# Kernel tuning notes

Hardware: AMD Instinct MI355X
Metric: run time of the kernel (lower is better)

Reference implementation:

```python
import jax, jax.numpy as jnp
import numpy as np

N, TC, K, TK, D, V = 64, 256, 32, 64, 256, 32000


def setup_inputs() -> dict:
    key = jax.random.key(0)
    k1, k2, k3, k4 = jax.random.split(key, 4)
    src_tokens = jax.random.randint(k1, (N, TC), 0, V)
    know_tokens = jax.random.randint(k2, (N, K, TK), 0, V)
    ck_mask = jnp.ones((N, K), dtype=bool)
    cs_ids = jax.random.randint(k3, (N,), 0, K)
    embed = jax.random.normal(k4, (V, D), dtype=jnp.float32)
    return {
        "src_tokens": src_tokens,
        "know_tokens": know_tokens,
        "ck_mask": ck_mask,
        "cs_ids": cs_ids,
        "use_cs_ids": 0,
        "embed": embed,
    }


def reference(src_tokens, know_tokens, ck_mask, cs_ids, use_cs_ids, embed):
    d = embed.shape[1]
    # "transformer" stand-in: embedding lookup; pad token 0 defines ragged mask
    ctx_enc = embed[src_tokens]                         # [N,Tc,D]
    ctx_mask = src_tokens != 0                          # [N,Tc]
    know_enc = embed[know_tokens]                       # [N,K,Tk,D]
    know_mask = (know_tokens != 0) & ck_mask[:, :, None]  # [N,K,Tk]

    ctx_len = ctx_mask.sum(-1)                          # [N]
    know_len = know_mask.sum(-1)                        # [N,K]

    # ragged segment-sum pooling with sqrt(D * length) normalization
    ctx_use = (ctx_enc * ctx_mask[..., None]).sum(1)
    ctx_use = ctx_use / jnp.sqrt(d * jnp.maximum(ctx_len, 1).astype(ctx_use.dtype))[:, None]
    know_use = (know_enc * know_mask[..., None]).sum(2)
    know_use = know_use / jnp.sqrt(d * jnp.maximum(know_len, 1).astype(know_use.dtype))[..., None]

    # batched mv attention: score per knowledge sentence
    ck_attn = jnp.einsum('nkd,nd->nk', know_use, ctx_use)  # [N,K]

    if use_cs_ids:
        cs = cs_ids
    else:
        cs = jnp.argmax(jnp.where(ck_mask, ck_attn, -jnp.inf), axis=1)

    ck_attn = jnp.where(ck_mask, ck_attn, 0.0)          # padded like to_tensor_mask

    # gather selected knowledge span
    cs_enc = jnp.take_along_axis(know_enc, cs[:, None, None, None], axis=1)[:, 0]   # [N,Tk,D]
    cs_mask = jnp.take_along_axis(know_mask, cs[:, None, None], axis=1)[:, 0]       # [N,Tk]

    full_enc = jnp.concatenate([cs_enc, ctx_enc], axis=1)      # [N,Tk+Tc,D]
    full_mask = jnp.concatenate([cs_mask, ctx_mask], axis=1)   # [N,Tk+Tc]
    full_enc = full_enc * full_mask[..., None]                 # zero padding like to_tensor_mask
    return full_enc, full_mask, ck_attn
```

## Files before the change

### kernel.cpp

```cpp
#include <hip/hip_runtime.h>
#include <hip/hip_bf16.h>
#include <math.h>

#define N_  64
#define TC_ 256
#define K_  32
#define TK_ 64
#define D_  256
#define TF_ (TK_ + TC_)

__global__ void k0_zero(float* __restrict__ ctx_sum, int* __restrict__ ctx_len) {
    int idx = blockIdx.x * 256 + threadIdx.x;
    if (idx < N_ * D_) ctx_sum[idx] = 0.f;
    if (idx < N_)      ctx_len[idx] = 0;
}

__global__ __launch_bounds__(256) void k1_ctx(
        const int* __restrict__ src, const float* __restrict__ embed,
        float* __restrict__ out_enc, float* __restrict__ out_mask,
        float* __restrict__ ctx_sum, int* __restrict__ ctx_len) {
    const int n = blockIdx.x >> 3;
    const int c = blockIdx.x & 7;
    const int d = threadIdx.x;

    __shared__ int toks[32];
    if (d < 32) toks[d] = src[n * TC_ + c * 32 + d];
    __syncthreads();

    float acc = 0.f;
    #pragma unroll 4
    for (int tt = 0; tt < 32; ++tt) {
        const int tok = toks[tt];
        float v = 0.f;
        if (tok != 0) v = embed[(size_t)tok * D_ + d];
        out_enc[((size_t)n * TF_ + TK_ + c * 32 + tt) * D_ + d] = v;
        acc += v;
    }
    atomicAdd(&ctx_sum[n * D_ + d], acc);

    if (d < 32) {
        const int m = (toks[d] != 0);
        out_mask[n * TF_ + TK_ + c * 32 + d] = m ? 1.f : 0.f;
        if (m) atomicAdd(&ctx_len[n], 1);
    }
}

__global__ __launch_bounds__(256) void k2_know(
        const int* __restrict__ know, const int* __restrict__ ckm,
        const float* __restrict__ embed,
        const float* __restrict__ ctx_sum, const int* __restrict__ ctx_len,
        float* __restrict__ out_attn, float* __restrict__ ws_score) {
    const int n = blockIdx.x >> 5;
    const int k = blockIdx.x & (K_ - 1);
    const int d = threadIdx.x;

    __shared__ int   toks[TK_];
    __shared__ float red[4];

    const int ck = ckm[n * K_ + k];
    if (d < TK_) toks[d] = know[((size_t)n * K_ + k) * TK_ + d];
    __syncthreads();

    float acc = 0.f;
    if (ck) {
        #pragma unroll 8
        for (int t = 0; t < TK_; ++t) {
            const int tok = toks[t];
            if (tok != 0) acc += embed[(size_t)tok * D_ + d];
        }
    }

    int lk = 0;
    if (d < 64) {
        unsigned long long ball = __ballot(ck && (toks[d] != 0));
        lk = __popcll(ball);
    }

    float p = acc * ctx_sum[n * D_ + d];
    #pragma unroll
    for (int o = 32; o > 0; o >>= 1) p += __shfl_down(p, o, 64);
    if ((d & 63) == 0) red[d >> 6] = p;
    __syncthreads();

    if (d == 0) {
        const float dot = red[0] + red[1] + red[2] + red[3];
        int lc = ctx_len[n]; if (lc < 1) lc = 1;
        if (lk < 1) lk = 1;
        const float score =
            dot / (sqrtf((float)D_ * (float)lc) * sqrtf((float)D_ * (float)lk));
        out_attn[n * K_ + k] = ck ? score : 0.f;
        ws_score[n * K_ + k] = ck ? score : -INFINITY;
    }
}

__global__ __launch_bounds__(256) void k3_sel(
        const int* __restrict__ know, const int* __restrict__ ckm,
        const int* __restrict__ cs_ids, const int* __restrict__ use_flag,
        const float* __restrict__ embed, const float* __restrict__ ws_score,
        float* __restrict__ out_enc, float* __restrict__ out_mask) {
    const int n = blockIdx.x >> 2;
    const int c = blockIdx.x & 3;
    const int d = threadIdx.x;

    int cs = 0;
    if (use_flag[0]) {
        cs = cs_ids[n];
    } else {
        float best = -INFINITY;
        #pragma unroll
        for (int j = 0; j < K_; ++j) {
            const float s = ws_score[n * K_ + j];
            if (s > best) { best = s; cs = j; }
        }
    }
    const int ck = ckm[n * K_ + cs];

    __shared__ int toks[16];
    if (d < 16) toks[d] = know[((size_t)n * K_ + cs) * TK_ + c * 16 + d];
    __syncthreads();

    #pragma unroll
    for (int tt = 0; tt < 16; ++tt) {
        const int tok = toks[tt];
        const int m = ck && (tok != 0);
        float v = 0.f;
        if (m) v = embed[(size_t)tok * D_ + d];
        out_enc[((size_t)n * TF_ + c * 16 + tt) * D_ + d] = v;
    }
    if (d < 16) {
        const int m = ck && (toks[d] != 0);
        out_mask[n * TF_ + c * 16 + d] = m ? 1.f : 0.f;
    }
}

extern "C" void kernel_launch(void* const* d_in, const int* in_sizes, int n_in,
                              void* d_out, int out_size, void* d_ws, size_t ws_size,
                              hipStream_t stream) {
    const int*   src      = (const int*)d_in[0];
    const int*   know     = (const int*)d_in[1];
    const int*   ckm      = (const int*)d_in[2];
    const int*   cs_ids   = (const int*)d_in[3];
    const int*   use_flag = (const int*)d_in[4];
    const float* embed    = (const float*)d_in[5];

    float* out      = (float*)d_out;
    float* out_enc  = out;
    float* out_mask = out + (size_t)N_ * TF_ * D_;
    float* out_attn = out_mask + (size_t)N_ * TF_;

    float* ctx_sum  = (float*)d_ws;
    int*   ctx_len  = (int*)(ctx_sum + N_ * D_);
    float* ws_score = (float*)(ctx_len + N_);

    hipLaunchKernelGGL(k0_zero, dim3((N_ * D_ + 255) / 256), dim3(256), 0, stream,
                       ctx_sum, ctx_len);
    hipLaunchKernelGGL(k1_ctx, dim3(N_ * 8), dim3(256), 0, stream,
                       src, embed, out_enc, out_mask, ctx_sum, ctx_len);
    hipLaunchKernelGGL(k2_know, dim3(N_ * K_), dim3(256), 0, stream,
                       know, ckm, embed, ctx_sum, ctx_len, out_attn, ws_score);
    hipLaunchKernelGGL(k3_sel, dim3(N_ * 4), dim3(256), 0, stream,
                       know, ckm, cs_ids, use_flag, embed, ws_score,
                       out_enc, out_mask);
}
```

Before: 130.5 us.

## Vectorize embedding gathers with float4 and replace atomics with per-chunk partials

Embedding rows are now gathered and written as float4, with each wave handling a subset of tokens across all 64 float4 lanes of a row. The zeroing kernel and the atomicAdd accumulation of context sums and lengths are replaced by per-chunk partial sums in workspace, which the knowledge kernel reduces itself. This removes one launch and atomic contention, and cuts the number of memory instructions. The cost is that every knowledge block re-reads eight partial vectors, and there is an extra shared-memory reduction in the context kernel.

```diff
diff --git a/kernel.cpp b/kernel.cpp
--- a/kernel.cpp
+++ b/kernel.cpp
@@ -1,5 +1,4 @@
 #include <hip/hip_runtime.h>
-#include <hip/hip_bf16.h>
 #include <math.h>
 
 #define N_  64
@@ -7,100 +6,125 @@
 #define K_  32
 #define TK_ 64
 #define D_  256
+#define D4_ (D_ / 4)
 #define TF_ (TK_ + TC_)
 
-__global__ void k0_zero(float* __restrict__ ctx_sum, int* __restrict__ ctx_len) {
-    int idx = blockIdx.x * 256 + threadIdx.x;
-    if (idx < N_ * D_) ctx_sum[idx] = 0.f;
-    if (idx < N_)      ctx_len[idx] = 0;
-}
-
-__global__ __launch_bounds__(256) void k1_ctx(
-        const int* __restrict__ src, const float* __restrict__ embed,
-        float* __restrict__ out_enc, float* __restrict__ out_mask,
-        float* __restrict__ ctx_sum, int* __restrict__ ctx_len) {
+__global__ __launch_bounds__(256) void kA_ctx(
+        const int* __restrict__ src, const float4* __restrict__ embed4,
+        float4* __restrict__ out_enc4, float* __restrict__ out_mask,
+        float4* __restrict__ ws_part4, int* __restrict__ ws_clen) {
     const int n = blockIdx.x >> 3;
     const int c = blockIdx.x & 7;
-    const int d = threadIdx.x;
+    const int tid = threadIdx.x;
+    const int w = tid >> 6, l = tid & 63;
 
     __shared__ int toks[32];
-    if (d < 32) toks[d] = src[n * TC_ + c * 32 + d];
+    __shared__ float4 part[4][64];
+
+    if (tid < 32) {
+        const int tok = src[n * TC_ + c * 32 + tid];
+        toks[tid] = tok;
+        out_mask[n * TF_ + TK_ + c * 32 + tid] = tok ? 1.f : 0.f;
+    }
     __syncthreads();
 
-    float acc = 0.f;
-    #pragma unroll 4
-    for (int tt = 0; tt < 32; ++tt) {
-        const int tok = toks[tt];
-        float v = 0.f;
-        if (tok != 0) v = embed[(size_t)tok * D_ + d];
-        out_enc[((size_t)n * TF_ + TK_ + c * 32 + tt) * D_ + d] = v;
-        acc += v;
+    float4 acc = {0.f, 0.f, 0.f, 0.f};
+    #pragma unroll
+    for (int i = 0; i < 8; ++i) {
+        const int t = w * 8 + i;
+        const int tok = toks[t];
+        float4 v = {0.f, 0.f, 0.f, 0.f};
+        if (tok) v = embed4[(size_t)tok * D4_ + l];
+        out_enc4[((size_t)n * TF_ + TK_ + c * 32 + t) * D4_ + l] = v;
+        acc.x += v.x; acc.y += v.y; acc.z += v.z; acc.w += v.w;
     }
-    atomicAdd(&ctx_sum[n * D_ + d], acc);
+    part[w][l] = acc;
+    __syncthreads();
 
-    if (d < 32) {
-        const int m = (toks[d] != 0);
-        out_mask[n * TF_ + TK_ + c * 32 + d] = m ? 1.f : 0.f;
-        if (m) atomicAdd(&ctx_len[n], 1);
+    if (w == 0) {
+        float4 a = part[0][l], b = part[1][l], p2 = part[2][l], p3 = part[3][l];
+        a.x += b.x + p2.x + p3.x;
+        a.y += b.y + p2.y + p3.y;
+        a.z += b.z + p2.z + p3.z;
+        a.w += b.w + p2.w + p3.w;
+        ws_part4[(size_t)(n * 8 + c) * D4_ + l] = a;
+        const unsigned long long ball = __ballot(l < 32 && toks[l] != 0);
+        if (l == 0) ws_clen[n * 8 + c] = __popcll(ball);
     }
 }
 
-__global__ __launch_bounds__(256) void k2_know(
+__global__ __launch_bounds__(256) void kB_know(
         const int* __restrict__ know, const int* __restrict__ ckm,
-        const float* __restrict__ embed,
-        const float* __restrict__ ctx_sum, const int* __restrict__ ctx_len,
+        const float4* __restrict__ embed4,
+        const float4* __restrict__ ws_part4, const int* __restrict__ ws_clen,
         float* __restrict__ out_attn, float* __restrict__ ws_score) {
     const int n = blockIdx.x >> 5;
     const int k = blockIdx.x & (K_ - 1);
-    const int d = threadIdx.x;
+    const int tid = threadIdx.x;
+    const int w = tid >> 6, l = tid & 63;
 
-    __shared__ int   toks[TK_];
-    __shared__ float red[4];
+    __shared__ int toks[TK_];
+    __shared__ float redp[4];
+    __shared__ int lk_sh;
+
+    if (tid < TK_) toks[tid] = know[((size_t)n * K_ + k) * TK_ + tid];
+    __syncthreads();
 
     const int ck = ckm[n * K_ + k];
-    if (d < TK_) toks[d] = know[((size_t)n * K_ + k) * TK_ + d];
-    __syncthreads();
 
-    float acc = 0.f;
+    float4 ctx = {0.f, 0.f, 0.f, 0.f};
+    #pragma unroll
+    for (int c = 0; c < 8; ++c) {
+        const float4 v = ws_part4[(size_t)(n * 8 + c) * D4_ + l];
+        ctx.x += v.x; ctx.y += v.y; ctx.z += v.z; ctx.w += v.w;
+    }
+
+    float4 acc = {0.f, 0.f, 0.f, 0.f};
     if (ck) {
-        #pragma unroll 8
-        for (int t = 0; t < TK_; ++t) {
-            const int tok = toks[t];
-            if (tok != 0) acc += embed[(size_t)tok * D_ + d];
+        #pragma unroll
+        for (int i = 0; i < 16; ++i) {
+            const int tok = toks[w * 16 + i];
+            if (tok) {
+                const float4 v = embed4[(size_t)tok * D4_ + l];
+                acc.x += v.x; acc.y += v.y; acc.z += v.z; acc.w += v.w;
+            }
         }
     }
 
-    int lk = 0;
-    if (d < 64) {
-        unsigned long long ball = __ballot(ck && (toks[d] != 0));
-        lk = __popcll(ball);
-    }
-
-    float p = acc * ctx_sum[n * D_ + d];
+    float p = acc.x * ctx.x + acc.y * ctx.y + acc.z * ctx.z + acc.w * ctx.w;
     #pragma unroll
     for (int o = 32; o > 0; o >>= 1) p += __shfl_down(p, o, 64);
-    if ((d & 63) == 0) red[d >> 6] = p;
+    if (l == 0) redp[w] = p;
+    if (w == 0) {
+        const unsigned long long ball = __ballot(toks[l] != 0);
+        if (l == 0) lk_sh = __popcll(ball);
+    }
     __syncthreads();
 
-    if (d == 0) {
-        const float dot = red[0] + red[1] + red[2] + red[3];
-        int lc = ctx_len[n]; if (lc < 1) lc = 1;
+    if (tid == 0) {
+        const float dot = redp[0] + redp[1] + redp[2] + redp[3];
+        int lc = 0;
+        #pragma unroll
+        for (int c = 0; c < 8; ++c) lc += ws_clen[n * 8 + c];
+        if (lc < 1) lc = 1;
+        int lk = ck ? lk_sh : 0;
         if (lk < 1) lk = 1;
         const float score =
-            dot / (sqrtf((float)D_ * (float)lc) * sqrtf((float)D_ * (float)lk));
+            dot / (sqrtf((float)(D_ * lc)) * sqrtf((float)(D_ * lk)));
         out_attn[n * K_ + k] = ck ? score : 0.f;
         ws_score[n * K_ + k] = ck ? score : -INFINITY;
     }
 }
 
-__global__ __launch_bounds__(256) void k3_sel(
+__global__ __launch_bounds__(256) void kC_sel(
         const int* __restrict__ know, const int* __restrict__ ckm,
         const int* __restrict__ cs_ids, const int* __restrict__ use_flag,
-        const float* __restrict__ embed, const float* __restrict__ ws_score,
-        float* __restrict__ out_enc, float* __restrict__ out_mask) {
+        const float4* __restrict__ embed4, const float* __restrict__ ws_score,
+        float4* __restrict__ out_enc4, float* __restrict__ out_mask) {
     const int n = blockIdx.x >> 2;
     const int c = blockIdx.x & 3;
-    const int d = threadIdx.x;
+    const int tid = threadIdx.x;
+    const int w = tid >> 6, l = tid & 63;
 
     int cs = 0;
     if (use_flag[0]) {
@@ -116,49 +140,47 @@
     const int ck = ckm[n * K_ + cs];
 
     __shared__ int toks[16];
-    if (d < 16) toks[d] = know[((size_t)n * K_ + cs) * TK_ + c * 16 + d];
+    if (tid < 16) {
+        const int tok = know[((size_t)n * K_ + cs) * TK_ + c * 16 + tid];
+        toks[tid] = tok;
+        out_mask[n * TF_ + c * 16 + tid] = (ck && tok) ? 1.f : 0.f;
+    }
     __syncthreads();
 
     #pragma unroll
-    for (int tt = 0; tt < 16; ++tt) {
-        const int tok = toks[tt];
-        const int m = ck && (tok != 0);
-        float v = 0.f;
-        if (m) v = embed[(size_t)tok * D_ + d];
-        out_enc[((size_t)n * TF_ + c * 16 + tt) * D_ + d] = v;
-    }
-    if (d < 16) {
-        const int m = ck && (toks[d] != 0);
-        out_mask[n * TF_ + c * 16 + d] = m ? 1.f : 0.f;
+    for (int i = 0; i < 4; ++i) {
+        const int t = w * 4 + i;
+        const int tok = toks[t];
+        float4 v = {0.f, 0.f, 0.f, 0.f};
+        if (ck && tok) v = embed4[(size_t)tok * D4_ + l];
+        out_enc4[((size_t)n * TF_ + c * 16 + t) * D4_ + l] = v;
     }
 }
 
 extern "C" void kernel_launch(void* const* d_in, const int* in_sizes, int n_in,
                               void* d_out, int out_size, void* d_ws, size_t ws_size,
                               hipStream_t stream) {
-    const int*   src      = (const int*)d_in[0];
-    const int*   know     = (const int*)d_in[1];
-    const int*   ckm      = (const int*)d_in[2];
-    const int*   cs_ids   = (const int*)d_in[3];
-    const int*   use_flag = (const int*)d_in[4];
-    const float* embed    = (const float*)d_in[5];
+    const int*    src      = (const int*)d_in[0];
+    const int*    know     = (const int*)d_in[1];
+    const int*    ckm      = (const int*)d_in[2];
+    const int*    cs_ids   = (const int*)d_in[3];
+    const int*    use_flag = (const int*)d_in[4];
+    const float4* embed4   = (const float4*)d_in[5];
 
-    float* out      = (float*)d_out;
-    float* out_enc  = out;
-    float* out_mask = out + (size_t)N_ * TF_ * D_;
-    float* out_attn = out_mask + (size_t)N_ * TF_;
+    float*  out      = (float*)d_out;
+    float4* out_enc4 = (float4*)out;
+    float*  out_mask = out + (size_t)N_ * TF_ * D_;
+    float*  out_attn = out_mask + (size_t)N_ * TF_;
 
-    float* ctx_sum  = (float*)d_ws;
-    int*   ctx_len  = (int*)(ctx_sum + N_ * D_);
-    float* ws_score = (float*)(ctx_len + N_);
+    float4* ws_part4 = (float4*)d_ws;
+    int*    ws_clen  = (int*)((float*)d_ws + (size_t)N_ * 8 * D_);
+    float*  ws_score = (float*)(ws_clen + N_ * 8);
 
-    hipLaunchKernelGGL(k0_zero, dim3((N_ * D_ + 255) / 256), dim3(256), 0, stream,
-                       ctx_sum, ctx_len);
-    hipLaunchKernelGGL(k1_ctx, dim3(N_ * 8), dim3(256), 0, stream,
-                       src, embed, out_enc, out_mask, ctx_sum, ctx_len);
-    hipLaunchKernelGGL(k2_know, dim3(N_ * K_), dim3(256), 0, stream,
-                       know, ckm, embed, ctx_sum, ctx_len, out_attn, ws_score);
-    hipLaunchKernelGGL(k3_sel, dim3(N_ * 4), dim3(256), 0, stream,
-                       know, ckm, cs_ids, use_flag, embed, ws_score,
-                       out_enc, out_mask);
+    hipLaunchKernelGGL(kA_ctx, dim3(N_ * 8), dim3(256), 0, stream,
+                       src, embed4, out_enc4, out_mask, ws_part4, ws_clen);
+    hipLaunchKernelGGL(kB_know, dim3(N_ * K_), dim3(256), 0, stream,
+                       know, ckm, embed4, ws_part4, ws_clen, out_attn, ws_score);
+    hipLaunchKernelGGL(kC_sel, dim3(N_ * 4), dim3(256), 0, stream,
+                       know, ckm, cs_ids, use_flag, embed4, ws_score,
+                       out_enc4, out_mask);
 }
```

Result: faster. 110.3 us (-15.5%).
